# Kernel optimization log

Hardware: AMD Instinct MI355X
Metric: run time of the kernel (lower is better)

The kernel has to match this reference:

```python
import jax, jax.numpy as jnp
import numpy as np

N = 4096  # number of training / query points
D_IN = 4  # input feature dim (fc1 in_features)
D_OUT = 3  # projected dim (fc1 out_features)


def setup_inputs() -> dict:
    key = jax.random.key(0)
    k1, k2, k3, k4 = jax.random.split(key, 4)
    x = jax.random.normal(k1, (N, D_IN), dtype=jnp.float32)
    # leave-one-out semantics require train_X to be the same points as x
    train_X = x
    Y = jax.random.normal(k2, (N, D_OUT), dtype=jnp.float32)
    W = jax.random.normal(k3, (D_OUT, D_IN), dtype=jnp.float32) * 0.5  # fc1.weight
    h = jnp.full((1,), 1.5, dtype=jnp.float32)  # learned bandwidth, init 1.5
    return {"x": x, "train_X": train_X, "Y": Y, "W": W, "h": h}


def reference(x, train_X, Y, W, h):
    # fc1 projections
    Fx = x @ W.T        # [N, 3]  Xw = fc1(x)
    Ft = train_X @ W.T  # [N, 3]  fc1(x_j) for all j
    # pairwise gaussian kernel: K[j, i, c] = exp(-((Ft[j,c]-Fx[i,c])/h)^2 / 2)
    d = (Ft[:, None, :] - Fx[None, :, :]) / h  # [N, N, 3]
    K = jnp.exp(-0.5 * d * d)
    # leave-one-out: tmp[j] = 0 zeroes the self-pair
    n = Fx.shape[0]
    K = K * (1.0 - jnp.eye(n, dtype=K.dtype))[:, :, None]
    denominator = K.sum(axis=0)                   # [N, 3]
    numerator = jnp.einsum('jic,jc->ic', K, Y)    # [N, 3]
    return numerator / denominator
```

## Files before the change

kernel.cpp:

```cpp
#include <hip/hip_runtime.h>
#include <hip/hip_bf16.h>


constexpr int TI  = 8;
constexpr int BLK = 256;

__global__ void proj_kernel(const float* __restrict__ x,
                            const float* __restrict__ tX,
                            const float* __restrict__ W,
                            float* __restrict__ F, int N) {
    int t = blockIdx.x * blockDim.x + threadIdx.x;
    if (t >= 2 * N) return;
    const float* src = (t < N) ? x : tX;
    int row = (t < N) ? t : t - N;
    float4 v = ((const float4*)src)[row];
#pragma unroll
    for (int c = 0; c < 3; ++c) {
        float s = v.x * W[c * 4 + 0] + v.y * W[c * 4 + 1] +
                  v.z * W[c * 4 + 2] + v.w * W[c * 4 + 3];
        F[t * 3 + c] = s;
    }
}

__global__ __launch_bounds__(BLK) void kde_main(const float* __restrict__ F,
                                                const float* __restrict__ Y,
                                                const float* __restrict__ hptr,
                                                float* __restrict__ out, int N) {
    const float* Fx = F;
    const float* Ft = F + 3 * N;
    const int i0  = blockIdx.x * TI;
    const int tid = threadIdx.x;

    const float h = hptr[0];
    const float scale = -0.72134752044448170368f / (h * h);

    float fx[TI][3];
#pragma unroll
    for (int a = 0; a < TI; ++a)
#pragma unroll
        for (int c = 0; c < 3; ++c) fx[a][c] = Fx[(i0 + a) * 3 + c];

    float num[TI][3], den[TI][3];
#pragma unroll
    for (int a = 0; a < TI; ++a)
#pragma unroll
        for (int c = 0; c < 3; ++c) { num[a][c] = 0.f; den[a][c] = 0.f; }

    for (int j = tid; j < N; j += BLK) {
        const float ft0 = Ft[3 * j + 0];
        const float ft1 = Ft[3 * j + 1];
        const float ft2 = Ft[3 * j + 2];
        const float y0  = Y[3 * j + 0];
        const float y1  = Y[3 * j + 1];
        const float y2  = Y[3 * j + 2];
#pragma unroll
        for (int a = 0; a < TI; ++a) {
            float d0 = ft0 - fx[a][0];
            float d1 = ft1 - fx[a][1];
            float d2 = ft2 - fx[a][2];
            float k0 = exp2f(scale * d0 * d0);
            float k1 = exp2f(scale * d1 * d1);
            float k2 = exp2f(scale * d2 * d2);
            den[a][0] += k0; num[a][0] = fmaf(k0, y0, num[a][0]);
            den[a][1] += k1; num[a][1] = fmaf(k1, y1, num[a][1]);
            den[a][2] += k2; num[a][2] = fmaf(k2, y2, num[a][2]);
        }
    }

#pragma unroll
    for (int a = 0; a < TI; ++a)
#pragma unroll
        for (int c = 0; c < 3; ++c) {
            float n_ = num[a][c], d_ = den[a][c];
#pragma unroll
            for (int off = 32; off > 0; off >>= 1) {
                n_ += __shfl_down(n_, off, 64);
                d_ += __shfl_down(d_, off, 64);
            }
            num[a][c] = n_; den[a][c] = d_;
        }

    __shared__ float s_num[4][TI * 3];
    __shared__ float s_den[4][TI * 3];
    const int lane = tid & 63, wave = tid >> 6;
    if (lane == 0) {
#pragma unroll
        for (int a = 0; a < TI; ++a)
#pragma unroll
            for (int c = 0; c < 3; ++c) {
                s_num[wave][a * 3 + c] = num[a][c];
                s_den[wave][a * 3 + c] = den[a][c];
            }
    }
    __syncthreads();

    if (tid < TI * 3) {
        float n_ = 0.f, d_ = 0.f;
#pragma unroll
        for (int w = 0; w < 4; ++w) { n_ += s_num[w][tid]; d_ += s_den[w][tid]; }
        const int a = tid / 3, c = tid - a * 3;
        const int i = i0 + a;
        float dd  = Ft[3 * i + c] - Fx[3 * i + c];
        float kii = exp2f(scale * dd * dd);
        n_ -= kii * Y[3 * i + c];
        d_ -= kii;
        out[3 * i + c] = n_ / d_;
    }
}

extern "C" void kernel_launch(void* const* d_in, const int* in_sizes, int n_in,
                              void* d_out, int out_size, void* d_ws, size_t ws_size,
                              hipStream_t stream) {
    const float* x  = (const float*)d_in[0];
    const float* tX = (const float*)d_in[1];
    const float* Y  = (const float*)d_in[2];
    const float* W  = (const float*)d_in[3];
    const float* h  = (const float*)d_in[4];

    const int N = in_sizes[0] / 4;
    float* F = (float*)d_ws;

    const int total = 2 * N;
    proj_kernel<<<(total + 255) / 256, 256, 0, stream>>>(x, tX, W, F, N);
    kde_main<<<N / TI, BLK, 0, stream>>>(F, Y, h, (float*)d_out, N);
}
```

Before: 83.69 us.

## Pack train projections with Y, compute query projections inline, use raw exp2

The projection kernel now only projects train_X and writes it, together with Y, as a 32-byte record per point. The main kernel reads each record with two float4 loads instead of six scalar loads. Query projections are computed inside the main kernel from x and W, so the Fx buffer is gone. The inner loop switches to the hardware exp2 builtin, which skips the libm wrapper's range handling. Block size and rows per block are halved and the j loop is unrolled, trading per-block reuse of each loaded record for more blocks in flight.

```diff
diff --git a/kernel.cpp b/kernel.cpp
--- a/kernel.cpp
+++ b/kernel.cpp
@@ -2,43 +2,48 @@
 #include <hip/hip_bf16.h>
 
 
-constexpr int TI  = 8;
-constexpr int BLK = 256;
+constexpr int BLK = 128;
+constexpr int TI  = 4;
 
-__global__ void proj_kernel(const float* __restrict__ x,
-                            const float* __restrict__ tX,
+__global__ void pack_kernel(const float* __restrict__ tX,
+                            const float* __restrict__ Y,
                             const float* __restrict__ W,
-                            float* __restrict__ F, int N) {
-    int t = blockIdx.x * blockDim.x + threadIdx.x;
-    if (t >= 2 * N) return;
-    const float* src = (t < N) ? x : tX;
-    int row = (t < N) ? t : t - N;
-    float4 v = ((const float4*)src)[row];
-#pragma unroll
-    for (int c = 0; c < 3; ++c) {
-        float s = v.x * W[c * 4 + 0] + v.y * W[c * 4 + 1] +
-                  v.z * W[c * 4 + 2] + v.w * W[c * 4 + 3];
-        F[t * 3 + c] = s;
-    }
+                            float* __restrict__ PK, int N) {
+    int j = blockIdx.x * blockDim.x + threadIdx.x;
+    if (j >= N) return;
+    float4 v = ((const float4*)tX)[j];
+    float f0 = v.x * W[0] + v.y * W[1] + v.z * W[2]  + v.w * W[3];
+    float f1 = v.x * W[4] + v.y * W[5] + v.z * W[6]  + v.w * W[7];
+    float f2 = v.x * W[8] + v.y * W[9] + v.z * W[10] + v.w * W[11];
+    float y0 = Y[3 * j + 0], y1 = Y[3 * j + 1], y2 = Y[3 * j + 2];
+    float4* o = (float4*)(PK + 8 * j);
+    o[0] = make_float4(f0, f1, f2, y0);
+    o[1] = make_float4(y1, y2, 0.f, 0.f);
 }
 
-__global__ __launch_bounds__(BLK) void kde_main(const float* __restrict__ F,
-                                                const float* __restrict__ Y,
+__global__ __launch_bounds__(BLK) void kde_main(const float* __restrict__ x,
+                                                const float* __restrict__ W,
+                                                const float* __restrict__ PK,
                                                 const float* __restrict__ hptr,
                                                 float* __restrict__ out, int N) {
-    const float* Fx = F;
-    const float* Ft = F + 3 * N;
     const int i0  = blockIdx.x * TI;
     const int tid = threadIdx.x;
 
     const float h = hptr[0];
     const float scale = -0.72134752044448170368f / (h * h);
 
+    float w[12];
+#pragma unroll
+    for (int k = 0; k < 12; ++k) w[k] = W[k];
+
     float fx[TI][3];
 #pragma unroll
-    for (int a = 0; a < TI; ++a)
-#pragma unroll
-        for (int c = 0; c < 3; ++c) fx[a][c] = Fx[(i0 + a) * 3 + c];
+    for (int a = 0; a < TI; ++a) {
+        float4 v = ((const float4*)x)[i0 + a];
+        fx[a][0] = v.x * w[0] + v.y * w[1] + v.z * w[2]  + v.w * w[3];
+        fx[a][1] = v.x * w[4] + v.y * w[5] + v.z * w[6]  + v.w * w[7];
+        fx[a][2] = v.x * w[8] + v.y * w[9] + v.z * w[10] + v.w * w[11];
+    }
 
     float num[TI][3], den[TI][3];
 #pragma unroll
@@ -46,24 +51,22 @@
 #pragma unroll
         for (int c = 0; c < 3; ++c) { num[a][c] = 0.f; den[a][c] = 0.f; }
 
+    const float4* PK4 = (const float4*)PK;
+#pragma unroll 4
     for (int j = tid; j < N; j += BLK) {
-        const float ft0 = Ft[3 * j + 0];
-        const float ft1 = Ft[3 * j + 1];
-        const float ft2 = Ft[3 * j + 2];
-        const float y0  = Y[3 * j + 0];
-        const float y1  = Y[3 * j + 1];
-        const float y2  = Y[3 * j + 2];
+        float4 p0 = PK4[2 * j + 0];
+        float4 p1 = PK4[2 * j + 1];
 #pragma unroll
         for (int a = 0; a < TI; ++a) {
-            float d0 = ft0 - fx[a][0];
-            float d1 = ft1 - fx[a][1];
-            float d2 = ft2 - fx[a][2];
-            float k0 = exp2f(scale * d0 * d0);
-            float k1 = exp2f(scale * d1 * d1);
-            float k2 = exp2f(scale * d2 * d2);
-            den[a][0] += k0; num[a][0] = fmaf(k0, y0, num[a][0]);
-            den[a][1] += k1; num[a][1] = fmaf(k1, y1, num[a][1]);
-            den[a][2] += k2; num[a][2] = fmaf(k2, y2, num[a][2]);
+            float d0 = p0.x - fx[a][0];
+            float d1 = p0.y - fx[a][1];
+            float d2 = p0.z - fx[a][2];
+            float k0 = __builtin_amdgcn_exp2f(scale * d0 * d0);
+            float k1 = __builtin_amdgcn_exp2f(scale * d1 * d1);
+            float k2 = __builtin_amdgcn_exp2f(scale * d2 * d2);
+            den[a][0] += k0; num[a][0] = fmaf(k0, p0.w, num[a][0]);
+            den[a][1] += k1; num[a][1] = fmaf(k1, p1.x, num[a][1]);
+            den[a][2] += k2; num[a][2] = fmaf(k2, p1.y, num[a][2]);
         }
     }
 
@@ -80,31 +83,30 @@
             num[a][c] = n_; den[a][c] = d_;
         }
 
-    __shared__ float s_num[4][TI * 3];
-    __shared__ float s_den[4][TI * 3];
+    __shared__ float s_n[2][TI * 3];
+    __shared__ float s_d[2][TI * 3];
     const int lane = tid & 63, wave = tid >> 6;
     if (lane == 0) {
 #pragma unroll
         for (int a = 0; a < TI; ++a)
 #pragma unroll
             for (int c = 0; c < 3; ++c) {
-                s_num[wave][a * 3 + c] = num[a][c];
-                s_den[wave][a * 3 + c] = den[a][c];
+                s_n[wave][a * 3 + c] = num[a][c];
+                s_d[wave][a * 3 + c] = den[a][c];
             }
     }
     __syncthreads();
 
     if (tid < TI * 3) {
-        float n_ = 0.f, d_ = 0.f;
-#pragma unroll
-        for (int w = 0; w < 4; ++w) { n_ += s_num[w][tid]; d_ += s_den[w][tid]; }
-        const int a = tid / 3, c = tid - a * 3;
+        const int a = tid / 3, c = tid - 3 * a;
         const int i = i0 + a;
-        float dd  = Ft[3 * i + c] - Fx[3 * i + c];
-        float kii = exp2f(scale * dd * dd);
-        n_ -= kii * Y[3 * i + c];
-        d_ -= kii;
-        out[3 * i + c] = n_ / d_;
+        float n_ = s_n[0][tid] + s_n[1][tid];
+        float d_ = s_d[0][tid] + s_d[1][tid];
+        float ft = PK[8 * i + c];
+        float y  = PK[8 * i + 3 + c];
+        float dd = ft - fx[a][c];
+        float kii = __builtin_amdgcn_exp2f(scale * dd * dd);
+        out[3 * i + c] = (n_ - kii * y) / (d_ - kii);
     }
 }
 
@@ -118,9 +120,8 @@
     const float* h  = (const float*)d_in[4];
 
     const int N = in_sizes[0] / 4;
-    float* F = (float*)d_ws;
+    float* PK = (float*)d_ws;
 
-    const int total = 2 * N;
-    proj_kernel<<<(total + 255) / 256, 256, 0, stream>>>(x, tX, W, F, N);
-    kde_main<<<N / TI, BLK, 0, stream>>>(F, Y, h, (float*)d_out, N);
+    pack_kernel<<<(N + 255) / 256, 256, 0, stream>>>(tX, Y, W, PK, N);
+    kde_main<<<N / TI, BLK, 0, stream>>>(x, W, PK, h, (float*)d_out, N);
 }
```

New measurement: 90.43 us. +8.1%, slower.

## Fuse projection into KDE kernel and expand squared-distance exponent algebraically

Applied to the files above, without the earlier changes.

Drops the separate projection kernel and its workspace round trip. Each block now projects its own query rows and the training rows on the fly from x, train_X and W. The Gaussian exponent is expanded so each pair costs one FMA before the exp: the per-j term scale*ft^2 is hoisted and a per-query coefficient -2*scale*fx is precomputed. The constant scale*fx^2 factor is left out because it cancels in the numerator/denominator ratio. The raw hardware exp2 builtin replaces exp2f and the j loop is unrolled by two. The trade-off is recomputing the training projections in every block and weaker numerical stability from the unnormalised exponent, which also feeds the leave-one-out subtraction.

```diff
diff --git a/kernel.cpp b/kernel.cpp
--- a/kernel.cpp
+++ b/kernel.cpp
@@ -2,43 +2,37 @@
 #include <hip/hip_bf16.h>
 
 
+constexpr int BLK = 256;
 constexpr int TI  = 8;
-constexpr int BLK = 256;
 
-__global__ void proj_kernel(const float* __restrict__ x,
-                            const float* __restrict__ tX,
-                            const float* __restrict__ W,
-                            float* __restrict__ F, int N) {
-    int t = blockIdx.x * blockDim.x + threadIdx.x;
-    if (t >= 2 * N) return;
-    const float* src = (t < N) ? x : tX;
-    int row = (t < N) ? t : t - N;
-    float4 v = ((const float4*)src)[row];
-#pragma unroll
-    for (int c = 0; c < 3; ++c) {
-        float s = v.x * W[c * 4 + 0] + v.y * W[c * 4 + 1] +
-                  v.z * W[c * 4 + 2] + v.w * W[c * 4 + 3];
-        F[t * 3 + c] = s;
-    }
-}
-
-__global__ __launch_bounds__(BLK) void kde_main(const float* __restrict__ F,
-                                                const float* __restrict__ Y,
-                                                const float* __restrict__ hptr,
-                                                float* __restrict__ out, int N) {
-    const float* Fx = F;
-    const float* Ft = F + 3 * N;
+__global__ __launch_bounds__(BLK) void kde_fused(const float* __restrict__ x,
+                                                 const float* __restrict__ tX,
+                                                 const float* __restrict__ Y,
+                                                 const float* __restrict__ W,
+                                                 const float* __restrict__ hptr,
+                                                 float* __restrict__ out, int N) {
     const int i0  = blockIdx.x * TI;
     const int tid = threadIdx.x;
 
     const float h = hptr[0];
     const float scale = -0.72134752044448170368f / (h * h);
 
-    float fx[TI][3];
+    float w[12];
 #pragma unroll
-    for (int a = 0; a < TI; ++a)
+    for (int k = 0; k < 12; ++k) w[k] = W[k];
+
+    float w2[TI][3];
 #pragma unroll
-        for (int c = 0; c < 3; ++c) fx[a][c] = Fx[(i0 + a) * 3 + c];
+    for (int a = 0; a < TI; ++a) {
+        float4 xv = ((const float4*)x)[i0 + a];
+#pragma unroll
+        for (int c = 0; c < 3; ++c) {
+            float fx = fmaf(xv.x, w[4 * c + 0],
+                       fmaf(xv.y, w[4 * c + 1],
+                       fmaf(xv.z, w[4 * c + 2], xv.w * w[4 * c + 3])));
+            w2[a][c] = -2.f * scale * fx;
+        }
+    }
 
     float num[TI][3], den[TI][3];
 #pragma unroll
@@ -46,27 +40,34 @@
 #pragma unroll
         for (int c = 0; c < 3; ++c) { num[a][c] = 0.f; den[a][c] = 0.f; }
 
+#pragma unroll 2
     for (int j = tid; j < N; j += BLK) {
-        const float ft0 = Ft[3 * j + 0];
-        const float ft1 = Ft[3 * j + 1];
-        const float ft2 = Ft[3 * j + 2];
-        const float y0  = Y[3 * j + 0];
-        const float y1  = Y[3 * j + 1];
-        const float y2  = Y[3 * j + 2];
+        float4 tv = ((const float4*)tX)[j];
+        float yv[3];
+        yv[0] = Y[3 * j + 0]; yv[1] = Y[3 * j + 1]; yv[2] = Y[3 * j + 2];
+        float ft[3], A[3];
 #pragma unroll
-        for (int a = 0; a < TI; ++a) {
-            float d0 = ft0 - fx[a][0];
-            float d1 = ft1 - fx[a][1];
-            float d2 = ft2 - fx[a][2];
-            float k0 = exp2f(scale * d0 * d0);
-            float k1 = exp2f(scale * d1 * d1);
-            float k2 = exp2f(scale * d2 * d2);
-            den[a][0] += k0; num[a][0] = fmaf(k0, y0, num[a][0]);
-            den[a][1] += k1; num[a][1] = fmaf(k1, y1, num[a][1]);
-            den[a][2] += k2; num[a][2] = fmaf(k2, y2, num[a][2]);
+        for (int c = 0; c < 3; ++c) {
+            ft[c] = fmaf(tv.x, w[4 * c + 0],
+                    fmaf(tv.y, w[4 * c + 1],
+                    fmaf(tv.z, w[4 * c + 2], tv.w * w[4 * c + 3])));
+            float v = scale * ft[c];
+            A[c] = v * ft[c];
         }
+#pragma unroll
+        for (int a = 0; a < TI; ++a)
+#pragma unroll
+            for (int c = 0; c < 3; ++c) {
+                float arg = fmaf(w2[a][c], ft[c], A[c]);
+                float k   = __builtin_amdgcn_exp2f(arg);
+                den[a][c] += k;
+                num[a][c]  = fmaf(k, yv[c], num[a][c]);
+            }
     }
 
+    __shared__ float s_n[4][TI * 3];
+    __shared__ float s_d[4][TI * 3];
+    const int lane = tid & 63, wave = tid >> 6;
 #pragma unroll
     for (int a = 0; a < TI; ++a)
 #pragma unroll
@@ -77,34 +78,31 @@
                 n_ += __shfl_down(n_, off, 64);
                 d_ += __shfl_down(d_, off, 64);
             }
-            num[a][c] = n_; den[a][c] = d_;
+            if (lane == 0) { s_n[wave][a * 3 + c] = n_; s_d[wave][a * 3 + c] = d_; }
         }
-
-    __shared__ float s_num[4][TI * 3];
-    __shared__ float s_den[4][TI * 3];
-    const int lane = tid & 63, wave = tid >> 6;
-    if (lane == 0) {
-#pragma unroll
-        for (int a = 0; a < TI; ++a)
-#pragma unroll
-            for (int c = 0; c < 3; ++c) {
-                s_num[wave][a * 3 + c] = num[a][c];
-                s_den[wave][a * 3 + c] = den[a][c];
-            }
-    }
     __syncthreads();
 
     if (tid < TI * 3) {
-        float n_ = 0.f, d_ = 0.f;
-#pragma unroll
-        for (int w = 0; w < 4; ++w) { n_ += s_num[w][tid]; d_ += s_den[w][tid]; }
-        const int a = tid / 3, c = tid - a * 3;
+        const int a = tid / 3, c = tid - 3 * a;
         const int i = i0 + a;
-        float dd  = Ft[3 * i + c] - Fx[3 * i + c];
-        float kii = exp2f(scale * dd * dd);
-        n_ -= kii * Y[3 * i + c];
-        d_ -= kii;
-        out[3 * i + c] = n_ / d_;
+        float n_ = s_n[0][tid] + s_n[1][tid] + s_n[2][tid] + s_n[3][tid];
+        float d_ = s_d[0][tid] + s_d[1][tid] + s_d[2][tid] + s_d[3][tid];
+
+        float4 xv = ((const float4*)x)[i];
+        float fx = fmaf(xv.x, W[4 * c + 0],
+                   fmaf(xv.y, W[4 * c + 1],
+                   fmaf(xv.z, W[4 * c + 2], xv.w * W[4 * c + 3])));
+        float w2v = -2.f * scale * fx;
+        float4 tv = ((const float4*)tX)[i];
+        float ft = fmaf(tv.x, W[4 * c + 0],
+                   fmaf(tv.y, W[4 * c + 1],
+                   fmaf(tv.z, W[4 * c + 2], tv.w * W[4 * c + 3])));
+        float v  = scale * ft;
+        float A  = v * ft;
+        float kii = __builtin_amdgcn_exp2f(fmaf(w2v, ft, A));
+        float yii = Y[3 * i + c];
+
+        out[3 * i + c] = (n_ - kii * yii) / (d_ - kii);
     }
 }
 
@@ -118,9 +116,6 @@
     const float* h  = (const float*)d_in[4];
 
     const int N = in_sizes[0] / 4;
-    float* F = (float*)d_ws;
 
-    const int total = 2 * N;
-    proj_kernel<<<(total + 255) / 256, 256, 0, stream>>>(x, tX, W, F, N);
-    kde_main<<<N / TI, BLK, 0, stream>>>(F, Y, h, (float*)d_out, N);
+    kde_fused<<<N / TI, BLK, 0, stream>>>(x, tX, Y, W, h, (float*)d_out, N);
 }
```

Result: faster. 77.09 us (-7.9%).
